# Performance work log

Measured on AMD Instinct MI355X. Metric: run time of the kernel, lower is better.

The kernel has to match this reference:

```python
import jax, jax.numpy as jnp
import numpy as np

B, L, V, D, H = 4096, 32, 50000, 300, 6
HD = D // H  # 50


def setup_inputs() -> dict:
    key = jax.random.key(0)
    ks = jax.random.split(key, 9)
    s = 0.02
    return {
        "title": jax.random.randint(ks[0], (B, L), 0, V),
        "emb": jax.random.normal(ks[1], (V, D), dtype=jnp.float32) * s,
        "pos_emb": jax.random.normal(ks[2], (512, D), dtype=jnp.float32) * s,
        "Wq": jax.random.normal(ks[3], (D, D), dtype=jnp.float32) * s,
        "bq": jnp.zeros((D,), jnp.float32),
        "Wk": jax.random.normal(ks[4], (D, D), dtype=jnp.float32) * s,
        "bk": jnp.zeros((D,), jnp.float32),
        "Wv": jax.random.normal(ks[5], (D, D), dtype=jnp.float32) * s,
        "bv": jnp.zeros((D,), jnp.float32),
        "Wo": jax.random.normal(ks[6], (D, D), dtype=jnp.float32) * s,
        "bo": jnp.zeros((D,), jnp.float32),
        "Va": jax.random.normal(ks[7], (D, D), dtype=jnp.float32) * s,
        "ba": jnp.zeros((D,), jnp.float32),
        "qw": jax.random.normal(ks[8], (D, 1), dtype=jnp.float32) * s,
    }


def reference(title, emb, pos_emb, Wq, bq, Wk, bk, Wv, bv, Wo, bo, Va, ba, qw):
    b, l = title.shape
    # word embedding + positional embedding
    x = emb[title] + pos_emb[:l][None, :, :]  # [B, L, D]

    def heads(y):  # [B, L, D] -> [B, H, L, HD]
        return y.reshape(b, l, H, HD).transpose(0, 2, 1, 3)

    # manual multi-head self-attention (mask is all-ones -> no masking effect)
    q = heads(x @ Wq.T + bq) / jnp.sqrt(jnp.float32(HD))
    k = heads(x @ Wk.T + bk)
    v = heads(x @ Wv.T + bv)
    scores = jnp.einsum("bhqd,bhkd->bhqk", q, k)  # [B, H, L, L]
    w = jax.nn.softmax(scores, axis=-1)  # dropout is identity in eval
    ctx = jnp.einsum("bhqk,bhkd->bhqd", w, v)
    ctx = ctx.transpose(0, 2, 1, 3).reshape(b, l, D)
    ctx = ctx @ Wo.T + bo  # [B, L, D]

    # additive attention pooling
    t = jnp.tanh(ctx @ Va.T + ba)          # [B, L, D]
    a = (t @ qw)[..., 0]                    # [B, L]
    alpha = jax.nn.softmax(a, axis=1)       # [B, L]
    out = jnp.einsum("bs,bsd->bd", alpha, ctx)  # [B, D]
    return out
```

## Files before the change

kernel.cpp:

```cpp
#include <hip/hip_runtime.h>
#include <math.h>

typedef _Float16 f16;
typedef _Float16 half8 __attribute__((ext_vector_type(8)));
typedef _Float16 half4 __attribute__((ext_vector_type(4)));
typedef float float4v __attribute__((ext_vector_type(4)));
typedef int int4v __attribute__((ext_vector_type(4)));

#define MFMA16(a, b, c) __builtin_amdgcn_mfma_f32_16x16x32_f16((a), (b), (c), 0, 0, 0)


#define WQKV_OFF 0u
#define BQKV_OFF 655360u
#define WO_OFF   659456u
#define WVA_OFF  864256u
#define BVA_OFF  1069056u
#define CBAR_OFF 1070336u

__device__ __forceinline__ float fast_tanh(float x) {
    float e = __expf(2.f * x);
    return 1.f - 2.f / (e + 1.f);
}

__global__ __launch_bounds__(256) void repack_all(
    const float* __restrict__ Wq, const float* __restrict__ Wk,
    const float* __restrict__ Wv, const float* __restrict__ Wo,
    const float* __restrict__ bq, const float* __restrict__ bk,
    const float* __restrict__ bv, const float* __restrict__ Va,
    const float* __restrict__ bo, const float* __restrict__ ba,
    f16* __restrict__ wqkvF, f16* __restrict__ wo16F, float* __restrict__ bqkv,
    f16* __restrict__ wvaF, float* __restrict__ bva) {
    const int bid = blockIdx.x, tid = threadIdx.x;
    const float rs = 0.14142135623730951f;
    if (bid < 1684) {
        int idx = bid * 256 + tid;
        if (idx < 327680) {
            int ntile = idx / 5120, rem = idx - ntile * 5120;
            int ks = rem / 512, r2 = rem - ks * 512;
            int lane = r2 >> 3, j = r2 & 7;
            int n = ntile * 16 + (lane & 15);
            int k = ks * 32 + (lane >> 4) * 8 + j;
            int g = n / 320, r = n - g * 320;
            float v = 0.f;
            if (r < 300 && k < 300) {
                if (g == 0) v = Wq[r * 300 + k] * rs;
                else if (g == 1) v = Wk[r * 300 + k];
                else if (g == 2) v = Wv[r * 300 + k];
            }
            wqkvF[idx] = (f16)v;
        } else if (idx < 430080) {
            int t = idx - 327680;
            int ntile = t / 5120, rem = t - ntile * 5120;
            int ks = rem / 512, r2 = rem - ks * 512;
            int lane = r2 >> 3, j = r2 & 7;
            int n = ntile * 16 + (lane & 15);
            int k = ks * 32 + (lane >> 4) * 8 + j;
            wo16F[t] = (f16)((n < 300 && k < 300) ? Wo[n * 300 + k] : 0.f);
        } else if (idx < 431104) {
            int n = idx - 430080;
            int g = n / 320, r = n - g * 320;
            float v = 0.f;
            if (r < 300) {
                if (g == 0) v = bq[r] * rs;
                else if (g == 1) v = bk[r];
                else if (g == 2) v = bv[r];
            }
            bqkv[n] = v;
        }
    } else if (bid < 1784) {
        int bt = (bid - 1684) * 4 + (tid >> 6);
        int mt = bt / 20, nt = bt % 20;
        int lane = tid & 63;
        int lr = lane & 15, quad = lane >> 4;
        float4v acc = {0.f, 0.f, 0.f, 0.f};
        int m = mt * 16 + lr;
        int nn = nt * 16 + lr;
        for (int ks = 0; ks < 10; ++ks) {
            int c = ks * 32 + quad * 8;
            half8 af, bf;
#pragma unroll
            for (int j = 0; j < 8; ++j) {
                int cc = c + j;
                af[j] = (f16)((m < 300 && cc < 300) ? Va[m * 300 + cc] : 0.f);
                bf[j] = (f16)((nn < 300 && cc < 300) ? Wo[cc * 300 + nn] : 0.f);
            }
            acc = MFMA16(af, bf, acc);
        }
#pragma unroll
        for (int r = 0; r < 4; ++r) {
            int row = mt * 16 + quad * 4 + r;
            int col = nt * 16 + lr;
            int addr = ((row >> 4) * 10 + (col >> 5)) * 512 +
                       (((col >> 3) & 3) * 16 + (row & 15)) * 8 + (col & 7);
            wvaF[addr] = (f16)acc[r];
        }
    } else {
        int j = (bid - 1784) * 4 + (tid >> 6);
        int lane = tid & 63;
        float s = 0.f;
        if (j < 300) {
            for (int k = lane; k < 300; k += 64) s += Va[j * 300 + k] * bo[k];
        }
#pragma unroll
        for (int off = 1; off < 64; off <<= 1) s += __shfl_xor(s, off, 64);
        if (lane == 0) bva[j] = (j < 300) ? s + ba[j] : 0.f;
    }
}

__global__ __launch_bounds__(512, 4) void qkvattn_kernel(
    const int* __restrict__ title, const float* __restrict__ emb,
    const float* __restrict__ pos,
    const f16* __restrict__ wqkvF, const float* __restrict__ bqkv,
    const f16* __restrict__ wvaF, const float* __restrict__ bva,
    const float* __restrict__ qw, f16* __restrict__ cbar) {
    __shared__ __align__(16) f16 qL[6 * 32 * 72];
    __shared__ __align__(16) f16 kL[6 * 32 * 72];
    __shared__ __align__(16) f16 vT[6 * 64 * 32];
    __shared__ float aL[32];
    const int ib = blockIdx.x, tid = threadIdx.x;
    const int w = tid >> 6, lane = tid & 63, lr = lane & 15, quad = lane >> 4;
    const float4v vz = {0.f, 0.f, 0.f, 0.f};
    const int4v z4 = {0, 0, 0, 0};
    f16* xA = vT;

    for (int u = tid; u < 1280; u += 512) {
        int fragblk = u >> 6, lu = u & 63;
        int mt = fragblk / 10, ks = fragblk - mt * 10;
        int row = mt * 16 + (lu & 15);
        int col = ks * 32 + (lu >> 4) * 8;
        int t = title[ib * 32 + row];
        half8 h;
        if (col + 8 <= 300) {
            float4v e0 = *(const float4v*)&emb[t * 300 + col];
            float4v e1 = *(const float4v*)&emb[t * 300 + col + 4];
            float4v p0 = *(const float4v*)&pos[row * 300 + col];
            float4v p1 = *(const float4v*)&pos[row * 300 + col + 4];
#pragma unroll
            for (int j = 0; j < 4; ++j) {
                h[j] = (f16)(e0[j] + p0[j]);
                h[4 + j] = (f16)(e1[j] + p1[j]);
            }
        } else {
#pragma unroll
            for (int j = 0; j < 8; ++j) {
                int cc = col + j;
                h[j] = (f16)((cc < 300) ? emb[t * 300 + cc] + pos[row * 300 + cc] : 0.f);
            }
        }
        *(half8*)&xA[u * 8] = h;
    }
    for (int i = tid; i < 1344; i += 512) {
        int hrow = i / 7, c = i - hrow * 7;
        ((int*)&qL[hrow * 72 + 50])[c] = 0;
        ((int*)&kL[hrow * 72 + 50])[c] = 0;
    }
    if (tid < 32) aL[tid] = 0.f;
    float bb[8];
#pragma unroll
    for (int j = 0; j < 8; ++j) bb[j] = bqkv[(w * 8 + j) * 16 + lr];
    __syncthreads();

    float4v acc[2][8];
#pragma unroll
    for (int mt = 0; mt < 2; ++mt)
#pragma unroll
        for (int j = 0; j < 8; ++j) acc[mt][j] = vz;
#pragma unroll
    for (int ks = 0; ks < 10; ++ks) {
        half8 a0 = *(const half8*)&xA[(ks * 64 + lane) * 8];
        half8 a1 = *(const half8*)&xA[((10 + ks) * 64 + lane) * 8];
#pragma unroll
        for (int j = 0; j < 8; ++j) {
            int tile = w * 8 + j;
            if (tile < 60) {
                half8 bf = *(const half8*)&wqkvF[((tile * 10 + ks) * 64 + lane) * 8];
                acc[0][j] = MFMA16(a0, bf, acc[0][j]);
                acc[1][j] = MFMA16(a1, bf, acc[1][j]);
            }
        }
    }
    __syncthreads();

    for (int i = tid; i < 336; i += 512) {
        int t = i >> 2, c4 = i & 3;
        int h = t / 14, d = 50 + (t - (t / 14) * 14);
        ((int4v*)&vT[(h * 64 + d) * 32])[c4] = z4;
    }
#pragma unroll
    for (int j = 0; j < 8; ++j) {
        int tile = w * 8 + j;
        int wi = tile / 20;
        int n = tile * 16 + lr;
        int cc = n - wi * 320;
        if (wi < 3 && cc < 300) {
            int h = cc / 50, d = cc - h * 50;
            if (wi == 2) {
#pragma unroll
                for (int mt = 0; mt < 2; ++mt) {
                    int row0 = mt * 16 + quad * 4;
                    half4 pk;
#pragma unroll
                    for (int r = 0; r < 4; ++r) pk[r] = (f16)(acc[mt][j][r] + bb[j]);
                    int idx = (h * 64 + d) * 32 + row0;
                    int byt = (idx * 2) ^ (((d >> 2) & 3) << 4);
                    *(half4*)((char*)vT + byt) = pk;
                }
            } else {
                f16* dst = (wi == 0) ? qL : kL;
#pragma unroll
                for (int mt = 0; mt < 2; ++mt)
#pragma unroll
                    for (int r = 0; r < 4; ++r) {
                        int row = mt * 16 + quad * 4 + r;
                        dst[(h * 32 + row) * 72 + d] = (f16)(acc[mt][j][r] + bb[j]);
                    }
            }
        }
    }
    __syncthreads();

    const int hh = w;
    if (w < 6) {
        float4v s00 = vz, s01 = vz, s10 = vz, s11 = vz;
#pragma unroll
        for (int ks = 0; ks < 2; ++ks) {
            int c = ks * 32 + quad * 8;
            half8 aq0 = *(const half8*)&qL[(hh * 32 + lr) * 72 + c];
            half8 aq1 = *(const half8*)&qL[(hh * 32 + 16 + lr) * 72 + c];
            half8 bk0 = *(const half8*)&kL[(hh * 32 + lr) * 72 + c];
            half8 bk1 = *(const half8*)&kL[(hh * 32 + 16 + lr) * 72 + c];
            s00 = MFMA16(aq0, bk0, s00);
            s01 = MFMA16(aq0, bk1, s01);
            s10 = MFMA16(aq1, bk0, s10);
            s11 = MFMA16(aq1, bk1, s11);
        }
        f16* ph = qL + hh * 32 * 72;
#pragma unroll
        for (int mt = 0; mt < 2; ++mt) {
            float4v sv0 = mt ? s10 : s00;
            float4v sv1 = mt ? s11 : s01;
#pragma unroll
            for (int r = 0; r < 4; ++r) {
                float v0 = sv0[r], v1 = sv1[r];
                float m = fmaxf(v0, v1);
#pragma unroll
                for (int off = 1; off < 16; off <<= 1) m = fmaxf(m, __shfl_xor(m, off, 64));
                float e0 = __expf(v0 - m), e1 = __expf(v1 - m);
                float ss = e0 + e1;
#pragma unroll
                for (int off = 1; off < 16; off <<= 1) ss += __shfl_xor(ss, off, 64);
                float inv = 1.0f / ss;
                int row = mt * 16 + quad * 4 + r;
                ph[row * 40 + lr] = (f16)(e0 * inv);
                ph[row * 40 + 16 + lr] = (f16)(e1 * inv);
            }
        }
    }
    __syncthreads();

    f16* scratch = kL;
    for (int i = tid; i < 32 * 28; i += 512) {
        int row = i / 28, cc = 300 + (i - row * 28);
        scratch[row * 328 + cc] = (f16)0.f;
    }
    if (w < 6) {
        int h = hh;
        f16* ph = qL + hh * 32 * 72;
        half8 aw0 = *(const half8*)&ph[lr * 40 + quad * 8];
        half8 aw1 = *(const half8*)&ph[(16 + lr) * 40 + quad * 8];
        float4v c0[4], c1[4];
#pragma unroll
        for (int nt = 0; nt < 4; ++nt) { c0[nt] = vz; c1[nt] = vz; }
#pragma unroll
        for (int nt = 0; nt < 4; ++nt) {
            int rIdx = nt * 16 + lr;
            int idx = (hh * 64 + rIdx) * 32 + quad * 8;
            int byt = (idx * 2) ^ (((rIdx >> 2) & 3) << 4);
            half8 bvf = *(const half8*)((const char*)vT + byt);
            c0[nt] = MFMA16(aw0, bvf, c0[nt]);
            c1[nt] = MFMA16(aw1, bvf, c1[nt]);
        }
#pragma unroll
        for (int mt = 0; mt < 2; ++mt)
#pragma unroll
            for (int nt = 0; nt < 4; ++nt)
#pragma unroll
                for (int r = 0; r < 4; ++r) {
                    int d = nt * 16 + lr;
                    if (d < 50) {
                        int row = mt * 16 + quad * 4 + r;
                        float4v cv = mt ? c1[nt] : c0[nt];
                        scratch[row * 328 + h * 50 + d] = (f16)cv[r];
                    }
                }
    }

    const int mtile = w >> 2, nsub = w & 3;
    half8 pbf[5];
    float pbva[5], pqw[5];
#pragma unroll
    for (int i = 0; i < 5; ++i) {
        int n = (nsub * 5 + i) * 16 + lr;
        pbf[i] = *(const half8*)&wvaF[(((nsub * 5 + i) * 10) * 64 + lane) * 8];
        pbva[i] = bva[n];
        pqw[i] = (n < 300) ? qw[n] : 0.f;
    }
    __syncthreads();

    {
        float4v vacc[5];
#pragma unroll
        for (int i = 0; i < 5; ++i) vacc[i] = vz;
        const int arow = (mtile * 16 + lr) * 328;
        {
            half8 a = *(const half8*)&scratch[arow + quad * 8];
#pragma unroll
            for (int i = 0; i < 5; ++i) vacc[i] = MFMA16(a, pbf[i], vacc[i]);
        }
#pragma unroll
        for (int ks = 1; ks < 10; ++ks) {
            half8 a = *(const half8*)&scratch[arow + ks * 32 + quad * 8];
#pragma unroll
            for (int i = 0; i < 5; ++i) {
                half8 bf = *(const half8*)&wvaF[((((nsub * 5 + i) * 10) + ks) * 64 + lane) * 8];
                vacc[i] = MFMA16(a, bf, vacc[i]);
            }
        }
        float ps[4] = {0.f, 0.f, 0.f, 0.f};
#pragma unroll
        for (int i = 0; i < 5; ++i) {
#pragma unroll
            for (int r = 0; r < 4; ++r) ps[r] += fast_tanh(vacc[i][r] + pbva[i]) * pqw[i];
        }
#pragma unroll
        for (int r = 0; r < 4; ++r)
#pragma unroll
            for (int off = 1; off < 16; off <<= 1) ps[r] += __shfl_xor(ps[r], off, 64);
        if (lr == 0) {
#pragma unroll
            for (int r = 0; r < 4; ++r) atomicAdd(&aL[mtile * 16 + quad * 4 + r], ps[r]);
        }
    }
    __syncthreads();

    {
        float av = aL[lane & 31];
        float m5 = av;
#pragma unroll
        for (int off = 1; off < 32; off <<= 1) m5 = fmaxf(m5, __shfl_xor(m5, off, 32));
        float e5 = __expf(av - m5);
        float ss5 = e5;
#pragma unroll
        for (int off = 1; off < 32; off <<= 1) ss5 += __shfl_xor(ss5, off, 32);
        float al = e5 / ss5;
        if (tid < 320) {
            int d = tid;
            float acc6 = 0.f;
#pragma unroll
            for (int l = 0; l < 32; ++l)
                acc6 += __shfl(al, l, 32) * (float)scratch[l * 328 + d];
            cbar[ib * 320 + d] = (f16)acc6;
        }
    }
}

__global__ __launch_bounds__(512) void out_kernel(
    const f16* __restrict__ cbar, const f16* __restrict__ wo16F,
    const float* __restrict__ bo, float* __restrict__ out) {
    __shared__ __align__(16) f16 cA[16 * 328];
    const int mb = blockIdx.x, tid = threadIdx.x;
    const int w = tid >> 6, lane = tid & 63, lr = lane & 15, quad = lane >> 4;
    for (int i = tid; i < 640; i += 512) {
        int row = i / 40, g = i - row * 40;
        *(half8*)&cA[row * 328 + g * 8] = *(const half8*)&cbar[(mb * 16 + row) * 320 + g * 8];
    }
    __syncthreads();
    const float4v vz = {0.f, 0.f, 0.f, 0.f};
    for (int t = w; t < 19; t += 8) {
        float4v acc = vz;
#pragma unroll
        for (int ks = 0; ks < 10; ++ks) {
            half8 a = *(const half8*)&cA[lr * 328 + ks * 32 + quad * 8];
            half8 bf = *(const half8*)&wo16F[((t * 10 + ks) * 64 + lane) * 8];
            acc = MFMA16(a, bf, acc);
        }
        int n = t * 16 + lr;
        if (n < 300) {
            float bb = bo[n];
#pragma unroll
            for (int r = 0; r < 4; ++r)
                out[(mb * 16 + quad * 4 + r) * 300 + n] = acc[r] + bb;
        }
    }
}

extern "C" void kernel_launch(void* const* d_in, const int* in_sizes, int n_in,
                              void* d_out, int out_size, void* d_ws, size_t ws_size,
                              hipStream_t stream) {
    const int* title = (const int*)d_in[0];
    const float* emb = (const float*)d_in[1];
    const float* pos = (const float*)d_in[2];
    const float* Wq = (const float*)d_in[3];
    const float* bq = (const float*)d_in[4];
    const float* Wk = (const float*)d_in[5];
    const float* bk = (const float*)d_in[6];
    const float* Wv = (const float*)d_in[7];
    const float* bv = (const float*)d_in[8];
    const float* Wo = (const float*)d_in[9];
    const float* bo = (const float*)d_in[10];
    const float* Va = (const float*)d_in[11];
    const float* ba = (const float*)d_in[12];
    const float* qw = (const float*)d_in[13];
    char* ws = (char*)d_ws;
    float* out = (float*)d_out;

    f16* wqkvF = (f16*)(ws + WQKV_OFF);
    float* bqkv = (float*)(ws + BQKV_OFF);
    f16* wo16F = (f16*)(ws + WO_OFF);
    f16* wvaF = (f16*)(ws + WVA_OFF);
    float* bva = (float*)(ws + BVA_OFF);
    f16* cbar = (f16*)(ws + CBAR_OFF);

    repack_all<<<1864, 256, 0, stream>>>(Wq, Wk, Wv, Wo, bq, bk, bv, Va, bo, ba,
                                         wqkvF, wo16F, bqkv, wvaF, bva);
    qkvattn_kernel<<<4096, 512, 0, stream>>>(title, emb, pos, wqkvF, bqkv, wvaF, bva,
                                             qw, cbar);
    out_kernel<<<256, 512, 0, stream>>>(cbar, wo16F, bo, out);
}
```

Baseline: 425.1 us.

## Vectorize weight repack, split Va·Wo fold over K, raise MFMA priority

The repack kernel now has each thread produce eight f16 values from two float4 loads and write them as one half8 store, instead of one scalar per thread. The Va·Wo product is split across four waves by K-slices and reduced through shared memory, so each 16x16 tile uses one block with short per-wave loops. The grid shrinks accordingly. The QKV MFMA loop in the main kernel is wrapped in s_setprio to favour matrix-issuing waves. The repack kernel is small next to the main kernel, so the possible saving is limited, and the priority hint could help or hurt scheduling.

```diff
diff --git a/kernel.cpp b/kernel.cpp
--- a/kernel.cpp
+++ b/kernel.cpp
@@ -30,34 +30,73 @@
     const float* __restrict__ bo, const float* __restrict__ ba,
     f16* __restrict__ wqkvF, f16* __restrict__ wo16F, float* __restrict__ bqkv,
     f16* __restrict__ wvaF, float* __restrict__ bva) {
+    __shared__ float4v red[4][64];
     const int bid = blockIdx.x, tid = threadIdx.x;
     const float rs = 0.14142135623730951f;
-    if (bid < 1684) {
-        int idx = bid * 256 + tid;
-        if (idx < 327680) {
-            int ntile = idx / 5120, rem = idx - ntile * 5120;
+    const float4v vz = {0.f, 0.f, 0.f, 0.f};
+    if (bid < 214) {
+        int s = bid * 256 + tid;
+        if (s < 40960) {
+            int a = s * 8;
+            int ntile = a / 5120, rem = a - ntile * 5120;
             int ks = rem / 512, r2 = rem - ks * 512;
-            int lane = r2 >> 3, j = r2 & 7;
+            int lane = r2 >> 3;
             int n = ntile * 16 + (lane & 15);
-            int k = ks * 32 + (lane >> 4) * 8 + j;
+            int k = ks * 32 + (lane >> 4) * 8;
             int g = n / 320, r = n - g * 320;
-            float v = 0.f;
-            if (r < 300 && k < 300) {
-                if (g == 0) v = Wq[r * 300 + k] * rs;
-                else if (g == 1) v = Wk[r * 300 + k];
-                else if (g == 2) v = Wv[r * 300 + k];
-            }
-            wqkvF[idx] = (f16)v;
-        } else if (idx < 430080) {
-            int t = idx - 327680;
-            int ntile = t / 5120, rem = t - ntile * 5120;
+            half8 h;
+#pragma unroll
+            for (int j = 0; j < 8; ++j) h[j] = (f16)0.f;
+            if (g < 3 && r < 300) {
+                const float* W = (g == 0) ? Wq : (g == 1) ? Wk : Wv;
+                float sc = (g == 0) ? rs : 1.f;
+                if (k + 8 <= 300) {
+                    float4v v0 = *(const float4v*)&W[r * 300 + k];
+                    float4v v1 = *(const float4v*)&W[r * 300 + k + 4];
+#pragma unroll
+                    for (int j = 0; j < 4; ++j) {
+                        h[j] = (f16)(v0[j] * sc);
+                        h[4 + j] = (f16)(v1[j] * sc);
+                    }
+                } else {
+#pragma unroll
+                    for (int j = 0; j < 8; ++j) {
+                        int kk = k + j;
+                        if (kk < 300) h[j] = (f16)(W[r * 300 + kk] * sc);
+                    }
+                }
+            }
+            *(half8*)&wqkvF[a] = h;
+        } else if (s < 53760) {
+            int a = (s - 40960) * 8;
+            int ntile = a / 5120, rem = a - ntile * 5120;
             int ks = rem / 512, r2 = rem - ks * 512;
-            int lane = r2 >> 3, j = r2 & 7;
+            int lane = r2 >> 3;
             int n = ntile * 16 + (lane & 15);
-            int k = ks * 32 + (lane >> 4) * 8 + j;
-            wo16F[t] = (f16)((n < 300 && k < 300) ? Wo[n * 300 + k] : 0.f);
-        } else if (idx < 431104) {
-            int n = idx - 430080;
+            int k = ks * 32 + (lane >> 4) * 8;
+            half8 h;
+#pragma unroll
+            for (int j = 0; j < 8; ++j) h[j] = (f16)0.f;
+            if (n < 300) {
+                if (k + 8 <= 300) {
+                    float4v v0 = *(const float4v*)&Wo[n * 300 + k];
+                    float4v v1 = *(const float4v*)&Wo[n * 300 + k + 4];
+#pragma unroll
+                    for (int j = 0; j < 4; ++j) {
+                        h[j] = (f16)v0[j];
+                        h[4 + j] = (f16)v1[j];
+                    }
+                } else {
+#pragma unroll
+                    for (int j = 0; j < 8; ++j) {
+                        int kk = k + j;
+                        if (kk < 300) h[j] = (f16)Wo[n * 300 + kk];
+                    }
+                }
+            }
+            *(half8*)&wo16F[a] = h;
+        } else if (s < 54784) {
+            int n = s - 53760;
             int g = n / 320, r = n - g * 320;
             float v = 0.f;
             if (r < 300) {
@@ -67,16 +106,18 @@
             }
             bqkv[n] = v;
         }
-    } else if (bid < 1784) {
-        int bt = (bid - 1684) * 4 + (tid >> 6);
-        int mt = bt / 20, nt = bt % 20;
-        int lane = tid & 63;
+    } else if (bid < 614) {
+        int bt = bid - 214;
+        int mt = bt / 20, nt = bt - mt * 20;
+        int w = tid >> 6, lane = tid & 63;
         int lr = lane & 15, quad = lane >> 4;
-        float4v acc = {0.f, 0.f, 0.f, 0.f};
         int m = mt * 16 + lr;
         int nn = nt * 16 + lr;
-        for (int ks = 0; ks < 10; ++ks) {
-            int c = ks * 32 + quad * 8;
+        float4v acc = vz;
+        int ks0 = (w < 2) ? w * 3 : 6 + (w - 2) * 2;
+        int ksn = (w < 2) ? 3 : 2;
+        for (int kk = 0; kk < ksn; ++kk) {
+            int c = (ks0 + kk) * 32 + quad * 8;
             half8 af, bf;
 #pragma unroll
             for (int j = 0; j < 8; ++j) {
@@ -86,16 +127,21 @@
             }
             acc = MFMA16(af, bf, acc);
         }
-#pragma unroll
-        for (int r = 0; r < 4; ++r) {
-            int row = mt * 16 + quad * 4 + r;
-            int col = nt * 16 + lr;
-            int addr = ((row >> 4) * 10 + (col >> 5)) * 512 +
-                       (((col >> 3) & 3) * 16 + (row & 15)) * 8 + (col & 7);
-            wvaF[addr] = (f16)acc[r];
+        red[w][lane] = acc;
+        __syncthreads();
+        if (w == 0) {
+            float4v s = red[0][lane] + red[1][lane] + red[2][lane] + red[3][lane];
+#pragma unroll
+            for (int r = 0; r < 4; ++r) {
+                int row = mt * 16 + quad * 4 + r;
+                int col = nt * 16 + lr;
+                int addr = ((row >> 4) * 10 + (col >> 5)) * 512 +
+                           (((col >> 3) & 3) * 16 + (row & 15)) * 8 + (col & 7);
+                wvaF[addr] = (f16)s[r];
+            }
         }
     } else {
-        int j = (bid - 1784) * 4 + (tid >> 6);
+        int j = (bid - 614) * 4 + (tid >> 6);
         int lane = tid & 63;
         float s = 0.f;
         if (j < 300) {
@@ -165,6 +211,7 @@
     for (int mt = 0; mt < 2; ++mt)
 #pragma unroll
         for (int j = 0; j < 8; ++j) acc[mt][j] = vz;
+    __builtin_amdgcn_s_setprio(1);
 #pragma unroll
     for (int ks = 0; ks < 10; ++ks) {
         half8 a0 = *(const half8*)&xA[(ks * 64 + lane) * 8];
@@ -179,6 +226,7 @@
             }
         }
     }
+    __builtin_amdgcn_s_setprio(0);
     __syncthreads();
 
     for (int i = tid; i < 336; i += 512) {
@@ -421,8 +469,8 @@
     float* bva = (float*)(ws + BVA_OFF);
     f16* cbar = (f16*)(ws + CBAR_OFF);
 
-    repack_all<<<1864, 256, 0, stream>>>(Wq, Wk, Wv, Wo, bq, bk, bv, Va, bo, ba,
-                                         wqkvF, wo16F, bqkv, wvaF, bva);
+    repack_all<<<694, 256, 0, stream>>>(Wq, Wk, Wv, Wo, bq, bk, bv, Va, bo, ba,
+                                        wqkvF, wo16F, bqkv, wvaF, bva);
     qkvattn_kernel<<<4096, 512, 0, stream>>>(title, emb, pos, wqkvF, bqkv, wvaF, bva,
                                              qw, cbar);
     out_kernel<<<256, 512, 0, stream>>>(cbar, wo16F, bo, out);
```

Result: faster. 402.9 us (-5.2%).
